# Optimization experiments

Measured on AMD Instinct MI355X. Metric: run time of the kernel, lower is better.

Reference implementation:

```python
import jax, jax.numpy as jnp
import numpy as np

B, N, IN, H, K, D, L = 8, 1024, 32, 32, 3, 16, 2  # batch, nodes, input_dim, hidden, cheb_k, embed_dim, layers


def setup_inputs() -> dict:
    key = jax.random.key(0)
    ks = jax.random.split(key, 4 + 4 * L)
    inp = {
        "xt": jax.random.normal(ks[0], (B, N, IN), jnp.float32),
        "init_state": jax.random.normal(ks[1], (L, B, N, H), jnp.float32),
        # row-normalized-ish support so the Chebyshev recursion stays bounded
        "support": jax.random.uniform(ks[2], (N, N), jnp.float32) / N,
        "embeddings": jax.random.normal(ks[3], (B, N, D), jnp.float32),
    }
    i = 4
    for l in range(L):
        cin = IN if l == 0 else H
        gi = K * (cin + H)
        inp[f"gate_w{l}"] = jax.random.normal(ks[i], (D, gi, 2 * H), jnp.float32) * (2.0 / (gi + 2 * H)) ** 0.5; i += 1
        inp[f"gate_b{l}"] = jax.random.normal(ks[i], (D, 2 * H), jnp.float32) * 0.05; i += 1
        inp[f"upd_w{l}"] = jax.random.normal(ks[i], (D, gi, H), jnp.float32) * (2.0 / (gi + H)) ** 0.5; i += 1
        inp[f"upd_b{l}"] = jax.random.normal(ks[i], (D, H), jnp.float32) * 0.05; i += 1
    return inp


def _cheb_gconv(x, support, emb, w_pool, b_pool):
    """HimGCN_share forward, meta_axis='ST', 2-D support.
    x: [B,N,C]; support: [N,N]; emb: [B,N,D];
    w_pool: [D, K*C, O]; b_pool: [D, O]. Returns [B,N,O]."""
    n = support.shape[0]
    graphs = [jnp.eye(n, dtype=x.dtype), support]
    for _ in range(2, K):
        graphs.append(2.0 * support @ graphs[-1] - graphs[-2])
    G = jnp.stack(graphs)                                   # [K,N,N]
    c = x.shape[-1]
    x_g = jnp.einsum('knm,bmc->bnkc', G, x).reshape(x.shape[0], n, K * c)  # concat over k
    # faithful to einsum('bni,bnio->bno') with bnio = einsum('bnd,dio->bnio'),
    # contracted in a memory-lighter order (same math)
    xe = jnp.einsum('bni,bnd->bnid', x_g, emb)              # [B,N,K*C,D]
    out = jnp.einsum('bnid,dio->bno', xe, w_pool)
    out = out + jnp.einsum('bnd,do->bno', emb, b_pool)
    return out


def _gcru_cell(x, state, support, emb, gw, gb, uw, ub):
    inp = jnp.concatenate([x, state], axis=-1)
    z_r = jax.nn.sigmoid(_cheb_gconv(inp, support, emb, gw, gb))
    z, r = z_r[..., :H], z_r[..., H:]
    cand = jnp.concatenate([x, z * state], axis=-1)
    hc = jnp.tanh(_cheb_gconv(cand, support, emb, uw, ub))
    return r * state + (1.0 - r) * hc


def reference(xt, init_state, support, embeddings,
              gate_w0, gate_b0, upd_w0, upd_b0,
              gate_w1, gate_b1, upd_w1, upd_b1):
    params = [(gate_w0, gate_b0, upd_w0, upd_b0), (gate_w1, gate_b1, upd_w1, upd_b1)]
    cur = xt
    hidden = []
    for l in range(L):
        gw, gb, uw, ub = params[l]
        cur = _gcru_cell(cur, init_state[l], support, embeddings, gw, gb, uw, ub)
        hidden.append(cur)
    return cur, jnp.stack(hidden)
```

## Files before the change

### kernel.cpp

```cpp
#include <hip/hip_runtime.h>
#include <math.h>

#define BB 8
#define NN 1024
#define HH 32
#define II 192
#define DD 16
#define BN (BB*NN)
#define MT 16
#define FR 512

typedef __attribute__((ext_vector_type(8))) short short8v;
typedef __attribute__((ext_vector_type(4))) float float4v;

union Frag8 { short8v v; uint2 u[2]; uint4 q; };

static __device__ inline ushort bf(float x) {
  union { float f; unsigned u; } c; c.f = x;
  unsigned r = c.u + 0x7FFFu + ((c.u >> 16) & 1u);
  return (ushort)(r >> 16);
}

static __device__ inline uint4 pack8(const ushort e[8]) {
  uint4 v;
  v.x = (unsigned)e[0] | ((unsigned)e[1] << 16);
  v.y = (unsigned)e[2] | ((unsigned)e[3] << 16);
  v.z = (unsigned)e[4] | ((unsigned)e[5] << 16);
  v.w = (unsigned)e[6] | ((unsigned)e[7] << 16);
  return v;
}

template <int O>
static __device__ void prep_w_frag(const float* __restrict__ W,
                                   ushort* __restrict__ WF, int d,
                                   float* lds)
{
  constexpr int NCG = O / 16;
  const float* Wd = W + (size_t)d * II * O;
  ushort* WFd = WF + (size_t)d * NCG * 6 * FR;
  const int tid = threadIdx.x;
  for (int f = tid; f < II * O / 4; f += 256) {
    int i = f / (O / 4);
    int o4 = (f % (O / 4)) * 4;
    float4 v = *(const float4*)(Wd + (size_t)i * O + o4);
    lds[i * (O + 1) + o4 + 0] = v.x; lds[i * (O + 1) + o4 + 1] = v.y;
    lds[i * (O + 1) + o4 + 2] = v.z; lds[i * (O + 1) + o4 + 3] = v.w;
  }
  __syncthreads();
  for (int f = tid; f < NCG * 6 * 64; f += 256) {
    int rem = f % 384;
    int ks = rem >> 6, l = rem & 63;
    int o = (f / 384) * 16 + (l & 15);
    int kb = ks * 32 + (l >> 4) * 4;
    ushort e[8];
#pragma unroll
    for (int j = 0; j < 4; ++j) {
      e[j] = bf(lds[(kb + j) * (O + 1) + o]);
      e[4 + j] = bf(lds[(kb + 16 + j) * (O + 1) + o]);
    }
    *(uint4*)(WFd + (size_t)f * 8) = pack8(e);
  }
}

__global__ __launch_bounds__(256) void prep_all(
    const float* __restrict__ S, ushort* __restrict__ Sb,
    ushort* __restrict__ SbF,
    const float* __restrict__ gw0, const float* __restrict__ gw1,
    ushort* __restrict__ wfg0, ushort* __restrict__ wfg1,
    const float* __restrict__ uw0, const float* __restrict__ uw1,
    ushort* __restrict__ wfu0, ushort* __restrict__ wfu1,
    const float* __restrict__ xt, const float* __restrict__ st0,
    const float* __restrict__ st1,
    ushort* __restrict__ xbTFg0, ushort* __restrict__ xbTFg1)
{
  __shared__ float ldsf[II * 65];
  int bx = blockIdx.x;
  const int tid = threadIdx.x;

  if (bx < 1024) {
    int idx = bx * 256 + tid;
    float4 v = ((const float4*)S)[idx];
    ushort4 o; o.x = bf(v.x); o.y = bf(v.y); o.z = bf(v.z); o.w = bf(v.w);
    ((ushort4*)Sb)[idx] = o;
    return;
  }
  bx -= 1024;
  if (bx < 32) {
    prep_w_frag<64>(bx >= 16 ? gw1 : gw0, bx >= 16 ? wfg1 : wfg0, bx & 15, ldsf);
    return;
  }
  bx -= 32;
  if (bx < 32) {
    prep_w_frag<32>(bx >= 16 ? uw1 : uw0, bx >= 16 ? wfu1 : wfu0, bx & 15, ldsf);
    return;
  }
  bx -= 32;
  if (bx < 384) {
    const int tensor = bx / 128, seg = bx % 128;
    const float* src = tensor == 0 ? xt : (tensor == 1 ? st0 : st1);
    ushort* T = (ushort*)ldsf;
    const int n0 = seg * 64;
#pragma unroll
    for (int q = 0; q < 2; ++q) {
      int f = tid + q * 256;
      int n = f >> 3, c4 = (f & 7) * 4;
      float4 v = *(const float4*)(src + (size_t)(n0 + n) * 32 + c4);
      T[(c4 + 0) * 72 + n] = bf(v.x); T[(c4 + 1) * 72 + n] = bf(v.y);
      T[(c4 + 2) * 72 + n] = bf(v.z); T[(c4 + 3) * 72 + n] = bf(v.w);
    }
    __syncthreads();
    {
      int gg = tid >> 7, ksl = (tid >> 6) & 1, l = tid & 63;
      int c = gg * 16 + (l & 15);
      int nb = ksl * 32 + (l >> 4) * 4;
      ushort e[8];
#pragma unroll
      for (int j = 0; j < 4; ++j) {
        e[j] = T[c * 72 + nb + j];
        e[4 + j] = T[c * 72 + nb + 16 + j];
      }
      int b = seg >> 4;
      int ks = (seg & 15) * 2 + ksl;
      ushort* dst; int g;
      if (tensor == 0)      { dst = xbTFg0; g = gg; }
      else if (tensor == 1) { dst = xbTFg0; g = 2 + gg; }
      else                  { dst = xbTFg1; g = 2 + gg; }
      *(uint4*)(dst + (((size_t)b * 4 + g) * 32 + ks) * FR + (size_t)l * 8) =
          pack8(e);
    }
    return;
  }
  bx -= 384;
  {
    const int mt = bx;
#pragma unroll
    for (int q = 0; q < 8; ++q) {
      int f = tid + q * 256;
      int ks = f >> 6, l = f & 63;
      int row = mt * 16 + (l & 15);
      int kb = ks * 32 + (l >> 4) * 4;
      float4 lo = *(const float4*)(S + (size_t)row * NN + kb);
      float4 hi = *(const float4*)(S + (size_t)row * NN + kb + 16);
      ushort e[8] = {bf(lo.x), bf(lo.y), bf(lo.z), bf(lo.w),
                     bf(hi.x), bf(hi.y), bf(hi.z), bf(hi.w)};
      *(uint4*)(SbF + ((size_t)mt * 32 + ks) * FR + (size_t)l * 8) = pack8(e);
    }
  }
}

__global__ __launch_bounds__(256) void prep_s2(
    const ushort* __restrict__ Sb, ushort* __restrict__ S2bF)
{
  __shared__ ushort A[32][136];
  __shared__ ushort Bt[32][132];
  __shared__ ushort C2[32][36];
  const int m0 = blockIdx.x * 32, n0 = blockIdx.y * 32;
  const int tid = threadIdx.x;
  const int w = tid >> 6, l = tid & 63;
  const int l15 = l & 15, l4 = l >> 4;
  const int wr = (w & 1) * 16, wc = (w >> 1) * 16;

  float4v acc = (float4v){0.f, 0.f, 0.f, 0.f};
  for (int k0 = 0; k0 < NN; k0 += 128) {
    __syncthreads();
#pragma unroll
    for (int q = 0; q < 2; ++q) {
      int f = tid + q * 256;
      int row = f >> 4, s8 = (f & 15) * 8;
      *(uint4*)&A[row][s8] = *(const uint4*)(Sb + (size_t)(m0 + row) * NN + k0 + s8);
    }
#pragma unroll
    for (int q = 0; q < 2; ++q) {
      int u = tid + q * 256;
      int kp = u >> 3, c4 = (u & 7) * 4;
      ushort4 a = *(const ushort4*)(Sb + (size_t)(k0 + 2 * kp) * NN + n0 + c4);
      ushort4 b = *(const ushort4*)(Sb + (size_t)(k0 + 2 * kp + 1) * NN + n0 + c4);
      *(unsigned*)&Bt[c4 + 0][2 * kp] = (unsigned)a.x | ((unsigned)b.x << 16);
      *(unsigned*)&Bt[c4 + 1][2 * kp] = (unsigned)a.y | ((unsigned)b.y << 16);
      *(unsigned*)&Bt[c4 + 2][2 * kp] = (unsigned)a.z | ((unsigned)b.z << 16);
      *(unsigned*)&Bt[c4 + 3][2 * kp] = (unsigned)a.w | ((unsigned)b.w << 16);
    }
    __syncthreads();
#pragma unroll
    for (int ks = 0; ks < 4; ++ks) {
      int kb = ks * 32 + l4 * 4;
      Frag8 af, bfr;
      af.u[0] = *(const uint2*)&A[wr + l15][kb];
      af.u[1] = *(const uint2*)&A[wr + l15][kb + 16];
      bfr.u[0] = *(const uint2*)&Bt[wc + l15][kb];
      bfr.u[1] = *(const uint2*)&Bt[wc + l15][kb + 16];
      acc = __builtin_amdgcn_mfma_f32_16x16x32_bf16(af.v, bfr.v, acc, 0, 0, 0);
    }
  }
  __syncthreads();
#pragma unroll
  for (int r = 0; r < 4; ++r)
    C2[wr + l4 * 4 + r][wc + l15] = bf(2.f * acc[r]);
  __syncthreads();
  if (tid < 128) {
    int fh = tid >> 6, l2 = tid & 63;
    ushort e[8];
#pragma unroll
    for (int j = 0; j < 4; ++j) {
      e[j] = C2[fh * 16 + (l2 & 15)][(l2 >> 4) * 4 + j];
      e[4 + j] = C2[fh * 16 + (l2 & 15)][(l2 >> 4) * 4 + 16 + j];
    }
    *(uint4*)(S2bF + ((size_t)(blockIdx.x * 2 + fh) * 32 + blockIdx.y) * FR +
              (size_t)l2 * 8) = pack8(e);
  }
}

template <int PHASE>
__global__ __launch_bounds__(256) void gconv_fused(
    const float* __restrict__ xb1,
    const float* __restrict__ xb2,
    const ushort* __restrict__ xbTF,
    const ushort* __restrict__ SbF,
    const ushort* __restrict__ S2bF,
    const float* __restrict__ emb,
    const ushort* __restrict__ WF,
    const float* __restrict__ bias,
    ushort* __restrict__ gT1c,
    float* __restrict__ gT2c,
    float* __restrict__ zr,
    float* __restrict__ zs,
    const float* __restrict__ state,
    float* __restrict__ hid,
    float* __restrict__ outp,
    ushort* __restrict__ xbTFout)
{
  constexpr int O = PHASE == 0 ? 64 : 32;
  constexpr int NCG = O / 16;
  __shared__ ushort A_sm[MT][200];
  __shared__ float emb_sm[MT][17];
  __shared__ float bias_sm[16][64];

  const int b = blockIdx.y;
  const int m0 = blockIdx.x * MT;
  const int tid = threadIdx.x;
  const int w = tid >> 6, l = tid & 63;
  const int l15 = l & 15, l4 = l >> 4;
  const int wcp = (PHASE == 0) ? w * 16 : (w & 1) * 16;

  if (tid < MT * 4) {
    int row = tid >> 2, d4 = (tid & 3) * 4;
    float4 v = *(const float4*)(emb + ((size_t)b * NN + m0 + row) * DD + d4);
    emb_sm[row][d4 + 0] = v.x; emb_sm[row][d4 + 1] = v.y;
    emb_sm[row][d4 + 2] = v.z; emb_sm[row][d4 + 3] = v.w;
  }
  for (int f = tid; f < DD * O / 4; f += 256) {
    int d = f / (O / 4), o4 = (f % (O / 4)) * 4;
    *(float4*)&bias_sm[d][o4] = *(const float4*)(bias + (size_t)d * O + o4);
  }
  {
    int row = tid >> 4, c4 = (tid & 15) * 4;
    const float* src = (c4 < 32) ? xb1 : xb2;
    float4 v = *(const float4*)(src + ((size_t)b * NN + m0 + row) * 32 + (c4 & 31));
    ushort4 o; o.x = bf(v.x); o.y = bf(v.y); o.z = bf(v.z); o.w = bf(v.w);
    *(ushort4*)&A_sm[row][c4] = o;
  }

  float4v acc1 = (float4v){0.f, 0.f, 0.f, 0.f};
  float4v acc2 = (float4v){0.f, 0.f, 0.f, 0.f};
  {
    const ushort* a1p = SbF + (size_t)blockIdx.x * 32 * FR + (size_t)l * 8;
    const ushort* a2p = S2bF + (size_t)blockIdx.x * 32 * FR + (size_t)l * 8;
    const ushort* bp = xbTF +
        (((size_t)b * NCG + (PHASE == 0 ? w : (w & 1))) * 32) * FR +
        (size_t)l * 8;
#pragma unroll 4
    for (int ks = 0; ks < 32; ++ks) {
      Frag8 a1, a2, b0;
      a1.q = *(const uint4*)(a1p + (size_t)ks * FR);
      a2.q = *(const uint4*)(a2p + (size_t)ks * FR);
      b0.q = *(const uint4*)(bp + (size_t)ks * FR);
      acc1 = __builtin_amdgcn_mfma_f32_16x16x32_bf16(a1.v, b0.v, acc1, 0, 0, 0);
      acc2 = __builtin_amdgcn_mfma_f32_16x16x32_bf16(a2.v, b0.v, acc2, 0, 0, 0);
    }
  }

  if (PHASE == 0 && w < 2) {
#pragma unroll
    for (int r = 0; r < 4; ++r) {
      size_t m = (size_t)b * NN + m0 + l4 * 4 + r;
      gT1c[m * 32 + wcp + l15] = bf(acc1[r]);
      gT2c[m * 32 + wcp + l15] = acc2[r];
    }
  }

  if (PHASE == 1) {
#pragma unroll
    for (int q = 0; q < 2; ++q) {
      int e = tid + q * 256;
      int row = e >> 5, c = e & 31;
      size_t m = (size_t)b * NN + m0 + row;
      A_sm[row][64 + c] = gT1c[m * 32 + c];
      A_sm[row][128 + c] = bf(gT2c[m * 32 + c] - xb1[m * 32 + c]);
    }
  }
  {
    const int colX = (PHASE == 0 ? 0 : 32) + wcp + l15;
    if (PHASE == 0 || w < 2) {
#pragma unroll
      for (int r = 0; r < 4; ++r) {
        int row = l4 * 4 + r;
        const float* src = (colX < 32) ? xb1 : xb2;
        float xv = src[((size_t)b * NN + m0 + row) * 32 + (colX & 31)];
        A_sm[row][64 + colX] = bf(acc1[r]);
        A_sm[row][128 + colX] = bf(acc2[r] - xv);
      }
    }
  }
  __syncthreads();

  const int cg = (PHASE == 0) ? w : (w & 1);
  const int ocol = cg * 16 + l15;
  const int erow = l4 * 4;
  const ushort* wfp = WF + (size_t)cg * 6 * FR + (size_t)l * 8;

  float4v outacc = (float4v){0.f, 0.f, 0.f, 0.f};

#pragma unroll 2
  for (int d = 0; d < DD; ++d) {
    const ushort* wpd = wfp + (size_t)d * NCG * 6 * FR;
    float4v acc = (float4v){0.f, 0.f, 0.f, 0.f};
#pragma unroll
    for (int ks = 0; ks < 6; ++ks) {
      int kb = ks * 32 + l4 * 4;
      Frag8 af, bfr;
      af.u[0] = *(const uint2*)&A_sm[l15][kb];
      af.u[1] = *(const uint2*)&A_sm[l15][kb + 16];
      bfr.q = *(const uint4*)(wpd + (size_t)ks * FR);
      acc = __builtin_amdgcn_mfma_f32_16x16x32_bf16(af.v, bfr.v, acc, 0, 0, 0);
    }
    float bb = bias_sm[d][ocol];
    outacc[0] += emb_sm[erow + 0][d] * (acc[0] + bb);
    outacc[1] += emb_sm[erow + 1][d] * (acc[1] + bb);
    outacc[2] += emb_sm[erow + 2][d] * (acc[2] + bb);
    outacc[3] += emb_sm[erow + 3][d] * (acc[3] + bb);
  }

  const int ksn = m0 >> 5;
  const int ebase = (m0 & 16) ? 4 : 0;
  const int lanep = l4 * 16 + (ocol & 15);

  if (PHASE == 0) {
    float zss[4];
#pragma unroll
    for (int r = 0; r < 4; ++r) {
      size_t m = (size_t)b * NN + m0 + erow + r;
      float zv = 1.f / (1.f + __expf(-outacc[r]));
      zr[m * 64 + ocol] = zv;
      if (ocol < 32) {
        float sv = zv * xb2[m * 32 + ocol];
        zs[m * 32 + ocol] = sv;
        zss[r] = sv;
      }
    }
    if (ocol < 32) {
      ushort4 pk; pk.x = bf(zss[0]); pk.y = bf(zss[1]);
      pk.z = bf(zss[2]); pk.w = bf(zss[3]);
      *(ushort4*)(xbTFout + (((size_t)b * 2 + (ocol >> 4)) * 32 + ksn) * FR +
                  (size_t)lanep * 8 + ebase) = pk;
    }
  } else if (w < 2) {
    float res[4];
#pragma unroll
    for (int r = 0; r < 4; ++r) {
      size_t m = (size_t)b * NN + m0 + erow + r;
      float hc = tanhf(outacc[r]);
      float rg = zr[m * 64 + 32 + ocol];
      float st = state[m * 32 + ocol];
      res[r] = rg * st + (1.f - rg) * hc;
      hid[m * 32 + ocol] = res[r];
      if (outp) outp[m * 32 + ocol] = res[r];
    }
    if (xbTFout) {
      ushort4 pk; pk.x = bf(res[0]); pk.y = bf(res[1]);
      pk.z = bf(res[2]); pk.w = bf(res[3]);
      *(ushort4*)(xbTFout + (((size_t)b * 4 + (ocol >> 4)) * 32 + ksn) * FR +
                  (size_t)lanep * 8 + ebase) = pk;
    }
  }
}

extern "C" void kernel_launch(void* const* d_in, const int* in_sizes, int n_in,
                              void* d_out, int out_size, void* d_ws, size_t ws_size,
                              hipStream_t stream)
{
  const float* xt         = (const float*)d_in[0];
  const float* init_state = (const float*)d_in[1];
  const float* S          = (const float*)d_in[2];
  const float* emb        = (const float*)d_in[3];

  float* out    = (float*)d_out;
  float* hidden = out + (size_t)BN * HH;

  float* zr   = (float*)d_ws;
  float* zs   = zr + (size_t)BN * 64;
  float* gT2c = zs + (size_t)BN * 32;
  ushort* gT1c = (ushort*)(gT2c + (size_t)BN * 32);
  ushort* Sb   = gT1c + (size_t)BN * 32;
  ushort* SbF  = Sb + (size_t)NN * NN;
  ushort* S2bF = SbF + (size_t)NN * NN;
  ushort* wfg0 = S2bF + (size_t)NN * NN;
  ushort* wfu0 = wfg0 + (size_t)DD * 4 * 6 * FR;
  ushort* wfg1 = wfu0 + (size_t)DD * 2 * 6 * FR;
  ushort* wfu1 = wfg1 + (size_t)DD * 4 * 6 * FR;
  ushort* xbTFg0 = wfu1 + (size_t)DD * 2 * 6 * FR;
  ushort* xbTFu0 = xbTFg0 + (size_t)BB * 4 * 32 * FR;
  ushort* xbTFg1 = xbTFu0 + (size_t)BB * 2 * 32 * FR;
  ushort* xbTFu1 = xbTFg1 + (size_t)BB * 4 * 32 * FR;

  const float* st0 = init_state;
  const float* st1 = init_state + (size_t)BN * HH;
  float* hid0 = hidden;
  float* hid1 = hidden + (size_t)BN * HH;

  prep_all<<<1536, 256, 0, stream>>>(
      S, Sb, SbF,
      (const float*)d_in[4], (const float*)d_in[8], wfg0, wfg1,
      (const float*)d_in[6], (const float*)d_in[10], wfu0, wfu1,
      xt, st0, st1, xbTFg0, xbTFg1);
  prep_s2<<<dim3(NN / 32, NN / 32), 256, 0, stream>>>(Sb, S2bF);

  dim3 g(NN / MT, BB);
  gconv_fused<0><<<g, 256, 0, stream>>>(
      xt, st0, xbTFg0, SbF, S2bF, emb, wfg0, (const float*)d_in[5],
      gT1c, gT2c, zr, zs, nullptr, nullptr, nullptr, xbTFu0);
  gconv_fused<1><<<g, 256, 0, stream>>>(
      xt, zs, xbTFu0, SbF, S2bF, emb, wfu0, (const float*)d_in[7],
      gT1c, gT2c, zr, nullptr, st0, hid0, nullptr, xbTFg1);
  gconv_fused<0><<<g, 256, 0, stream>>>(
      hid0, st1, xbTFg1, SbF, S2bF, emb, wfg1, (const float*)d_in[9],
      gT1c, gT2c, zr, zs, nullptr, nullptr, nullptr, xbTFu1);
  gconv_fused<1><<<g, 256, 0, stream>>>(
      hid0, zs, xbTFu1, SbF, S2bF, emb, wfu1, (const float*)d_in[11],
      gT1c, gT2c, zr, nullptr, st1, hid1, out, nullptr);
}
```

Baseline: 100.3 us.

## Fuse S^2 GEMM into prep kernel and swizzle gconv block mapping

Removes the separate bf16 copy of the support matrix and the standalone prep_s2 launch. The S·S product is now computed inside prep_all, converting fp32 S to bf16 on the fly while filling shared memory, and prep_all's shared memory becomes a union. The intent is to save one kernel launch and the write and re-read of a 2 MB intermediate. The gconv grid is also flattened to 1D with an interleaved tile index, possibly to change which blocks share cache. The trade-off is that the GEMM blocks now read fp32 S twice per element, and the S^2 work competes with the other prep blocks inside one launch.

Result: no change. 99.87 us (-0.5%).

```diff
diff --git a/kernel.cpp b/kernel.cpp
--- a/kernel.cpp
+++ b/kernel.cpp
@@ -63,8 +63,8 @@
 }
 
 __global__ __launch_bounds__(256) void prep_all(
-    const float* __restrict__ S, ushort* __restrict__ Sb,
-    ushort* __restrict__ SbF,
+    const float* __restrict__ S,
+    ushort* __restrict__ SbF, ushort* __restrict__ S2bF,
     const float* __restrict__ gw0, const float* __restrict__ gw1,
     ushort* __restrict__ wfg0, ushort* __restrict__ wfg1,
     const float* __restrict__ uw0, const float* __restrict__ uw1,
@@ -73,32 +73,93 @@
     const float* __restrict__ st1,
     ushort* __restrict__ xbTFg0, ushort* __restrict__ xbTFg1)
 {
-  __shared__ float ldsf[II * 65];
+  union PrepSm {
+    float wlds[II * 65];
+    struct { ushort A[32][136]; ushort Bt[32][132]; ushort C2[32][36]; } s2;
+    ushort T[32 * 72];
+  };
+  __shared__ PrepSm sm;
   int bx = blockIdx.x;
   const int tid = threadIdx.x;
 
   if (bx < 1024) {
-    int idx = bx * 256 + tid;
-    float4 v = ((const float4*)S)[idx];
-    ushort4 o; o.x = bf(v.x); o.y = bf(v.y); o.z = bf(v.z); o.w = bf(v.w);
-    ((ushort4*)Sb)[idx] = o;
+    const int m0 = (bx >> 5) * 32, n0 = (bx & 31) * 32;
+    const int w = tid >> 6, l = tid & 63;
+    const int l15 = l & 15, l4 = l >> 4;
+    const int wr = (w & 1) * 16, wc = (w >> 1) * 16;
+
+    float4v acc = (float4v){0.f, 0.f, 0.f, 0.f};
+    for (int k0 = 0; k0 < NN; k0 += 128) {
+      __syncthreads();
+#pragma unroll
+      for (int q = 0; q < 2; ++q) {
+        int f = tid + q * 256;
+        int row = f >> 4, s8 = (f & 15) * 8;
+        float4 lo = *(const float4*)(S + (size_t)(m0 + row) * NN + k0 + s8);
+        float4 hi = *(const float4*)(S + (size_t)(m0 + row) * NN + k0 + s8 + 4);
+        sm.s2.A[row][s8 + 0] = bf(lo.x); sm.s2.A[row][s8 + 1] = bf(lo.y);
+        sm.s2.A[row][s8 + 2] = bf(lo.z); sm.s2.A[row][s8 + 3] = bf(lo.w);
+        sm.s2.A[row][s8 + 4] = bf(hi.x); sm.s2.A[row][s8 + 5] = bf(hi.y);
+        sm.s2.A[row][s8 + 6] = bf(hi.z); sm.s2.A[row][s8 + 7] = bf(hi.w);
+      }
+#pragma unroll
+      for (int q = 0; q < 2; ++q) {
+        int u = tid + q * 256;
+        int kp = u >> 3, c4 = (u & 7) * 4;
+        float4 a = *(const float4*)(S + (size_t)(k0 + 2 * kp) * NN + n0 + c4);
+        float4 b = *(const float4*)(S + (size_t)(k0 + 2 * kp + 1) * NN + n0 + c4);
+        *(unsigned*)&sm.s2.Bt[c4 + 0][2 * kp] = (unsigned)bf(a.x) | ((unsigned)bf(b.x) << 16);
+        *(unsigned*)&sm.s2.Bt[c4 + 1][2 * kp] = (unsigned)bf(a.y) | ((unsigned)bf(b.y) << 16);
+        *(unsigned*)&sm.s2.Bt[c4 + 2][2 * kp] = (unsigned)bf(a.z) | ((unsigned)bf(b.z) << 16);
+        *(unsigned*)&sm.s2.Bt[c4 + 3][2 * kp] = (unsigned)bf(a.w) | ((unsigned)bf(b.w) << 16);
+      }
+      __syncthreads();
+#pragma unroll
+      for (int ks = 0; ks < 4; ++ks) {
+        int kb = ks * 32 + l4 * 4;
+        Frag8 af, bfr;
+        af.u[0] = *(const uint2*)&sm.s2.A[wr + l15][kb];
+        af.u[1] = *(const uint2*)&sm.s2.A[wr + l15][kb + 16];
+        bfr.u[0] = *(const uint2*)&sm.s2.Bt[wc + l15][kb];
+        bfr.u[1] = *(const uint2*)&sm.s2.Bt[wc + l15][kb + 16];
+        acc = __builtin_amdgcn_mfma_f32_16x16x32_bf16(af.v, bfr.v, acc, 0, 0, 0);
+      }
+    }
+    __syncthreads();
+#pragma unroll
+    for (int r = 0; r < 4; ++r)
+      sm.s2.C2[wr + l4 * 4 + r][wc + l15] = bf(2.f * acc[r]);
+    __syncthreads();
+    if (tid < 128) {
+      int fh = tid >> 6, l2 = tid & 63;
+      ushort e[8];
+#pragma unroll
+      for (int j = 0; j < 4; ++j) {
+        e[j] = sm.s2.C2[fh * 16 + (l2 & 15)][(l2 >> 4) * 4 + j];
+        e[4 + j] = sm.s2.C2[fh * 16 + (l2 & 15)][(l2 >> 4) * 4 + 16 + j];
+      }
+      *(uint4*)(S2bF + ((size_t)((bx >> 5) * 2 + fh) * 32 + (bx & 31)) * FR +
+                (size_t)l2 * 8) = pack8(e);
+    }
     return;
   }
   bx -= 1024;
   if (bx < 32) {
-    prep_w_frag<64>(bx >= 16 ? gw1 : gw0, bx >= 16 ? wfg1 : wfg0, bx & 15, ldsf);
+    prep_w_frag<64>(bx >= 16 ? gw1 : gw0, bx >= 16 ? wfg1 : wfg0, bx & 15,
+                    sm.wlds);
     return;
   }
   bx -= 32;
   if (bx < 32) {
-    prep_w_frag<32>(bx >= 16 ? uw1 : uw0, bx >= 16 ? wfu1 : wfu0, bx & 15, ldsf);
+    prep_w_frag<32>(bx >= 16 ? uw1 : uw0, bx >= 16 ? wfu1 : wfu0, bx & 15,
+                    sm.wlds);
     return;
   }
   bx -= 32;
   if (bx < 384) {
     const int tensor = bx / 128, seg = bx % 128;
     const float* src = tensor == 0 ? xt : (tensor == 1 ? st0 : st1);
-    ushort* T = (ushort*)ldsf;
+    ushort* T = sm.T;
     const int n0 = seg * 64;
 #pragma unroll
     for (int q = 0; q < 2; ++q) {
@@ -145,68 +206,6 @@
                      bf(hi.x), bf(hi.y), bf(hi.z), bf(hi.w)};
       *(uint4*)(SbF + ((size_t)mt * 32 + ks) * FR + (size_t)l * 8) = pack8(e);
     }
-  }
-}
-
-__global__ __launch_bounds__(256) void prep_s2(
-    const ushort* __restrict__ Sb, ushort* __restrict__ S2bF)
-{
-  __shared__ ushort A[32][136];
-  __shared__ ushort Bt[32][132];
-  __shared__ ushort C2[32][36];
-  const int m0 = blockIdx.x * 32, n0 = blockIdx.y * 32;
-  const int tid = threadIdx.x;
-  const int w = tid >> 6, l = tid & 63;
-  const int l15 = l & 15, l4 = l >> 4;
-  const int wr = (w & 1) * 16, wc = (w >> 1) * 16;
-
-  float4v acc = (float4v){0.f, 0.f, 0.f, 0.f};
-  for (int k0 = 0; k0 < NN; k0 += 128) {
-    __syncthreads();
-#pragma unroll
-    for (int q = 0; q < 2; ++q) {
-      int f = tid + q * 256;
-      int row = f >> 4, s8 = (f & 15) * 8;
-      *(uint4*)&A[row][s8] = *(const uint4*)(Sb + (size_t)(m0 + row) * NN + k0 + s8);
-    }
-#pragma unroll
-    for (int q = 0; q < 2; ++q) {
-      int u = tid + q * 256;
-      int kp = u >> 3, c4 = (u & 7) * 4;
-      ushort4 a = *(const ushort4*)(Sb + (size_t)(k0 + 2 * kp) * NN + n0 + c4);
-      ushort4 b = *(const ushort4*)(Sb + (size_t)(k0 + 2 * kp + 1) * NN + n0 + c4);
-      *(unsigned*)&Bt[c4 + 0][2 * kp] = (unsigned)a.x | ((unsigned)b.x << 16);
-      *(unsigned*)&Bt[c4 + 1][2 * kp] = (unsigned)a.y | ((unsigned)b.y << 16);
-      *(unsigned*)&Bt[c4 + 2][2 * kp] = (unsigned)a.z | ((unsigned)b.z << 16);
-      *(unsigned*)&Bt[c4 + 3][2 * kp] = (unsigned)a.w | ((unsigned)b.w << 16);
-    }
-    __syncthreads();
-#pragma unroll
-    for (int ks = 0; ks < 4; ++ks) {
-      int kb = ks * 32 + l4 * 4;
-      Frag8 af, bfr;
-      af.u[0] = *(const uint2*)&A[wr + l15][kb];
-      af.u[1] = *(const uint2*)&A[wr + l15][kb + 16];
-      bfr.u[0] = *(const uint2*)&Bt[wc + l15][kb];
-      bfr.u[1] = *(const uint2*)&Bt[wc + l15][kb + 16];
-      acc = __builtin_amdgcn_mfma_f32_16x16x32_bf16(af.v, bfr.v, acc, 0, 0, 0);
-    }
-  }
-  __syncthreads();
-#pragma unroll
-  for (int r = 0; r < 4; ++r)
-    C2[wr + l4 * 4 + r][wc + l15] = bf(2.f * acc[r]);
-  __syncthreads();
-  if (tid < 128) {
-    int fh = tid >> 6, l2 = tid & 63;
-    ushort e[8];
-#pragma unroll
-    for (int j = 0; j < 4; ++j) {
-      e[j] = C2[fh * 16 + (l2 & 15)][(l2 >> 4) * 4 + j];
-      e[4 + j] = C2[fh * 16 + (l2 & 15)][(l2 >> 4) * 4 + 16 + j];
-    }
-    *(uint4*)(S2bF + ((size_t)(blockIdx.x * 2 + fh) * 32 + blockIdx.y) * FR +
-              (size_t)l2 * 8) = pack8(e);
   }
 }
 
@@ -235,8 +234,10 @@
   __shared__ float emb_sm[MT][17];
   __shared__ float bias_sm[16][64];
 
-  const int b = blockIdx.y;
-  const int m0 = blockIdx.x * MT;
+  const int bid = blockIdx.x;
+  const int mt = (bid & 7) * 8 + ((bid >> 3) & 7);
+  const int b = bid >> 6;
+  const int m0 = mt * MT;
   const int tid = threadIdx.x;
   const int w = tid >> 6, l = tid & 63;
   const int l15 = l & 15, l4 = l >> 4;
@@ -263,8 +264,8 @@
   float4v acc1 = (float4v){0.f, 0.f, 0.f, 0.f};
   float4v acc2 = (float4v){0.f, 0.f, 0.f, 0.f};
   {
-    const ushort* a1p = SbF + (size_t)blockIdx.x * 32 * FR + (size_t)l * 8;
-    const ushort* a2p = S2bF + (size_t)blockIdx.x * 32 * FR + (size_t)l * 8;
+    const ushort* a1p = SbF + (size_t)mt * 32 * FR + (size_t)l * 8;
+    const ushort* a2p = S2bF + (size_t)mt * 32 * FR + (size_t)l * 8;
     const ushort* bp = xbTF +
         (((size_t)b * NCG + (PHASE == 0 ? w : (w & 1))) * 32) * FR +
         (size_t)l * 8;
@@ -400,8 +401,7 @@
   float* zs   = zr + (size_t)BN * 64;
   float* gT2c = zs + (size_t)BN * 32;
   ushort* gT1c = (ushort*)(gT2c + (size_t)BN * 32);
-  ushort* Sb   = gT1c + (size_t)BN * 32;
-  ushort* SbF  = Sb + (size_t)NN * NN;
+  ushort* SbF  = gT1c + (size_t)BN * 32;
   ushort* S2bF = SbF + (size_t)NN * NN;
   ushort* wfg0 = S2bF + (size_t)NN * NN;
   ushort* wfu0 = wfg0 + (size_t)DD * 4 * 6 * FR;
@@ -418,23 +418,21 @@
   float* hid1 = hidden + (size_t)BN * HH;
 
   prep_all<<<1536, 256, 0, stream>>>(
-      S, Sb, SbF,
+      S, SbF, S2bF,
       (const float*)d_in[4], (const float*)d_in[8], wfg0, wfg1,
       (const float*)d_in[6], (const float*)d_in[10], wfu0, wfu1,
       xt, st0, st1, xbTFg0, xbTFg1);
-  prep_s2<<<dim3(NN / 32, NN / 32), 256, 0, stream>>>(Sb, S2bF);
-
-  dim3 g(NN / MT, BB);
-  gconv_fused<0><<<g, 256, 0, stream>>>(
+
+  gconv_fused<0><<<512, 256, 0, stream>>>(
       xt, st0, xbTFg0, SbF, S2bF, emb, wfg0, (const float*)d_in[5],
       gT1c, gT2c, zr, zs, nullptr, nullptr, nullptr, xbTFu0);
-  gconv_fused<1><<<g, 256, 0, stream>>>(
+  gconv_fused<1><<<512, 256, 0, stream>>>(
       xt, zs, xbTFu0, SbF, S2bF, emb, wfu0, (const float*)d_in[7],
       gT1c, gT2c, zr, nullptr, st0, hid0, nullptr, xbTFg1);
-  gconv_fused<0><<<g, 256, 0, stream>>>(
+  gconv_fused<0><<<512, 256, 0, stream>>>(
       hid0, st1, xbTFg1, SbF, S2bF, emb, wfg1, (const float*)d_in[9],
       gT1c, gT2c, zr, zs, nullptr, nullptr, nullptr, xbTFu1);
-  gconv_fused<1><<<g, 256, 0, stream>>>(
+  gconv_fused<1><<<512, 256, 0, stream>>>(
       hid0, zs, xbTFu1, SbF, S2bF, emb, wfu1, (const float*)d_in[11],
       gT1c, gT2c, zr, nullptr, st1, hid1, out, nullptr);
 }
```
